# Optimization experiments

Measured on AMD Instinct MI355X. Metric: run time of the kernel, lower is better.

Reference implementation:

```python
import jax, jax.numpy as jnp
import numpy as np

QMAX = 127.0
QMIN = -128.0


def setup_inputs() -> dict:
    key = jax.random.key(0)
    k1, k2, k3 = jax.random.split(key, 3)
    B, N, D, O = 4, 4096, 2048, 2048
    x = jax.random.normal(k1, (B, N, D), dtype=jnp.float32)
    weight = jax.random.normal(k2, (O, D), dtype=jnp.float32)
    bias = jax.random.normal(k3, (O,), dtype=jnp.float32)
    return {"x": x, "weight": weight, "bias": bias}


def reference(x, weight, bias):
    # --- per-row symmetric int8 quantization of the weight [O, D] ---
    w_max = jnp.clip(jnp.max(jnp.abs(weight), axis=1, keepdims=True), 1e-8, None)
    w_scale = (w_max / QMAX)                     # [O, 1]
    w_q = jnp.clip(jnp.round(weight / w_scale), QMIN, QMAX).astype(jnp.int8)
    w_scale = w_scale.squeeze(1).astype(jnp.float32)  # [O]

    # --- dynamic per-row symmetric int8 quantization of x [B, N, D] ---
    x_max = jnp.max(jnp.abs(x), axis=2, keepdims=True)       # [B, N, 1]
    x_scale = jnp.maximum(x_max / QMAX, 1e-12)               # [B, N, 1]
    x_q = jnp.clip(jnp.round(x / x_scale), QMIN, QMAX).astype(jnp.int8)

    # --- int8 GEMM accumulated in int32: [B,N,D] x [O,D]^T -> [B,N,O] ---
    acc = jnp.einsum("bnd,od->bno", x_q.astype(jnp.int32), w_q.astype(jnp.int32))

    # --- dequantize with per-row activation scale and per-out-channel weight scale ---
    y = acc.astype(jnp.float32) * x_scale.astype(jnp.float32) * w_scale[None, None, :]
    y = y + bias
    return y.astype(x.dtype)
```

## Files before the change

kernel.cpp:

```cpp
#include <hip/hip_runtime.h>
#include <stdint.h>
#include <stddef.h>

typedef int v4i __attribute__((ext_vector_type(4)));

#define GLOAD_LDS16(g, l) __builtin_amdgcn_global_load_lds( \
    (const __attribute__((address_space(1))) void*)(g),     \
    (__attribute__((address_space(3))) void*)(l), 16, 0, 0)

__device__ __forceinline__ int pack4(float4 f, float s) {
    int a = (int)rintf(f.x / s); a = a < -128 ? -128 : (a > 127 ? 127 : a);
    int b = (int)rintf(f.y / s); b = b < -128 ? -128 : (b > 127 ? 127 : b);
    int c = (int)rintf(f.z / s); c = c < -128 ? -128 : (c > 127 ? 127 : c);
    int d = (int)rintf(f.w / s); d = d < -128 ? -128 : (d > 127 ? 127 : d);
    return (a & 255) | ((b & 255) << 8) | ((c & 255) << 16) | ((d & 255) << 24);
}

__global__ __launch_bounds__(256) void quant_both_2048(
    const float* __restrict__ x, signed char* __restrict__ xq,
    float* __restrict__ xs,
    const float* __restrict__ w, signed char* __restrict__ wq,
    float* __restrict__ wsc, int nx4)
{
    const int lane = threadIdx.x & 63;
    const bool isx = ((int)blockIdx.x < nx4);
    const int rb   = isx ? blockIdx.x : (blockIdx.x - nx4);
    const int row  = rb * 4 + (threadIdx.x >> 6);
    const float* in = isx ? x : w;
    signed char* q  = isx ? xq : wq;
    float* scales   = isx ? xs : wsc;
    const float floorv = isx ? 1e-12f : (1e-8f / 127.0f);
    const float* rp = in + (size_t)row * 2048;

    float4 v[8];
#pragma unroll
    for (int j = 0; j < 2; ++j) {
        const float4* p = (const float4*)(rp + j * 1024 + lane * 16);
#pragma unroll
        for (int i = 0; i < 4; ++i) v[j * 4 + i] = p[i];
    }
    float am = 0.0f;
#pragma unroll
    for (int i = 0; i < 8; ++i) {
        am = fmaxf(am, fabsf(v[i].x));
        am = fmaxf(am, fabsf(v[i].y));
        am = fmaxf(am, fabsf(v[i].z));
        am = fmaxf(am, fabsf(v[i].w));
    }
#pragma unroll
    for (int off = 32; off; off >>= 1) am = fmaxf(am, __shfl_xor(am, off));
    const float s = fmaxf(am / 127.0f, floorv);

#pragma unroll
    for (int j = 0; j < 2; ++j) {
        int4 pk;
        pk.x = pack4(v[j * 4 + 0], s);
        pk.y = pack4(v[j * 4 + 1], s);
        pk.z = pack4(v[j * 4 + 2], s);
        pk.w = pack4(v[j * 4 + 3], s);
        *(int4*)(q + (size_t)row * 2048 + j * 1024 + lane * 16) = pk;
    }
    if (lane == 0) scales[row] = s;
}

__global__ __launch_bounds__(256, 3) void gemm_i8_r3s(
    const signed char* __restrict__ xq, const signed char* __restrict__ wq,
    const float* __restrict__ xs, const float* __restrict__ ws,
    const float* __restrict__ bias, float* __restrict__ out, int K)
{
    __shared__ __align__(16) signed char lds[49152];

    const int tid  = threadIdx.x;
    const int lane = tid & 63;
    const int wid  = tid >> 6;
    const int wm   = wid >> 1;
    const int wn   = wid & 1;

    const int nwg  = gridDim.x * gridDim.y;
    int orig = blockIdx.y * gridDim.x + blockIdx.x;
    int swz  = ((nwg & 7) == 0) ? ((orig & 7) * (nwg >> 3) + (orig >> 3)) : orig;
    const int brow = (swz / gridDim.x) * 128;
    const int bcol = (swz % gridDim.x) * 128;

    const int gch = (((tid & 3) ^ ((tid >> 3) & 3)) << 4);
    const signed char* gA = xq + (size_t)(brow + (tid >> 2)) * K;
    const signed char* gB = wq + (size_t)(bcol + (tid >> 2)) * K;

#define ST4(tt, bb) do {                                                                  \
    GLOAD_LDS16(gA + (size_t)(tt) * 64 + gch,                  lds + (bb) * 16384 + (tid << 4));         \
    GLOAD_LDS16(gA + (size_t)64 * K + (size_t)(tt) * 64 + gch, lds + (bb) * 16384 + 4096 + (tid << 4));  \
    GLOAD_LDS16(gB + (size_t)(tt) * 64 + gch,                  lds + (bb) * 16384 + 8192 + (tid << 4));  \
    GLOAD_LDS16(gB + (size_t)64 * K + (size_t)(tt) * 64 + gch, lds + (bb) * 16384 + 12288 + (tid << 4)); \
} while (0)

    const int rl   = lane & 15;
    const int ko   = lane >> 4;
    const int slot = ((ko ^ ((rl >> 1) & 3)) << 4);

#define FRAG_A(bb, r) (*(const v4i*)(lds + (bb) * 16384 + (r) * 64 + slot))
#define FRAG_B(bb, r) (*(const v4i*)(lds + (bb) * 16384 + 8192 + (r) * 64 + slot))

    v4i acc[4][4] = {};
    const int ar = wm * 64 + rl;
    const int br = wn * 64 + rl;

    ST4(0, 0);
    ST4(1, 1);
    asm volatile("s_waitcnt vmcnt(4)" ::: "memory");
    __builtin_amdgcn_s_barrier();

    const int NT = K >> 6;
    for (int t = 0; t < NT; ++t) {
        const int buf = t % 3;

        v4i af[4], bf[4];
#pragma unroll
        for (int m = 0; m < 4; ++m) af[m] = FRAG_A(buf, ar + m * 16);
#pragma unroll
        for (int n = 0; n < 4; ++n) bf[n] = FRAG_B(buf, br + n * 16);

        if (t + 2 < NT) ST4(t + 2, (t + 2) % 3);

#pragma unroll
        for (int m = 0; m < 4; ++m)
#pragma unroll
            for (int n = 0; n < 4; ++n)
                acc[m][n] = __builtin_amdgcn_mfma_i32_16x16x64_i8(
                    af[m], bf[n], acc[m][n], 0, 0, 0);

        if (t + 2 < NT) {
            asm volatile("s_waitcnt vmcnt(4) lgkmcnt(0)" ::: "memory");
            __builtin_amdgcn_s_barrier();
        } else if (t + 2 == NT) {
            asm volatile("s_waitcnt vmcnt(0) lgkmcnt(0)" ::: "memory");
            __builtin_amdgcn_s_barrier();
        }
    }

    const int rg = lane >> 4;
#pragma unroll
    for (int n = 0; n < 4; ++n) {
        const int col = bcol + wn * 64 + n * 16 + rl;
        const float wsc = ws[col];
        const float bv  = bias[col];
#pragma unroll
        for (int m = 0; m < 4; ++m) {
#pragma unroll
            for (int j = 0; j < 4; ++j) {
                const int row = brow + wm * 64 + m * 16 + rg * 4 + j;
                out[(size_t)row * 2048 + col] =
                    (float)acc[m][n][j] * xs[row] * wsc + bv;
            }
        }
    }
#undef ST4
#undef FRAG_A
#undef FRAG_B
}

extern "C" void kernel_launch(void* const* d_in, const int* in_sizes, int n_in,
                              void* d_out, int out_size, void* d_ws, size_t ws_size,
                              hipStream_t stream) {
    const float* x    = (const float*)d_in[0];
    const float* w    = (const float*)d_in[1];
    const float* bias = (const float*)d_in[2];
    float* out = (float*)d_out;

    const int D = 2048;
    const int O = in_sizes[2];
    const int M = in_sizes[0] / D;

    char* wsb = (char*)d_ws;
    signed char* xq  = (signed char*)wsb;
    signed char* wqp = (signed char*)(wsb + (size_t)M * D);
    float* xs  = (float*)(wsb + (size_t)M * D + (size_t)O * D);
    float* wsc = (float*)(wsb + (size_t)M * D + (size_t)O * D + (size_t)M * 4);

    quant_both_2048<<<(M + O) / 4, 256, 0, stream>>>(x, xq, xs, w, wqp, wsc, M / 4);

    dim3 grid(O / 128, M / 128);
    gemm_i8_r3s<<<grid, 256, 0, stream>>>(xq, wqp, xs, wsc, bias, out, D);
}
```

Before: 131.1 us.

## Give each wave private LDS staging to eliminate block barriers in int8 GEMM

Each of the four waves now loads its own 64-row A and B slices into a private 32KB LDS region with a 4-stage ring, so no workgroup barriers are needed and only per-wave vmcnt waits gate consumption. Fragments are double-buffered in registers with the loop unrolled by two so that LDS reads overlap MFMAs. The cost is that A and B rows shared between waves are now loaded twice, which doubles global traffic per block, and the 128KB LDS footprint limits occupancy to one block per CU.

```diff
diff --git a/kernel.cpp b/kernel.cpp
--- a/kernel.cpp
+++ b/kernel.cpp
@@ -63,12 +63,12 @@
     if (lane == 0) scales[row] = s;
 }
 
-__global__ __launch_bounds__(256, 3) void gemm_i8_r3s(
+__global__ __launch_bounds__(256, 1) void gemm_i8_nobar(
     const signed char* __restrict__ xq, const signed char* __restrict__ wq,
     const float* __restrict__ xs, const float* __restrict__ ws,
     const float* __restrict__ bias, float* __restrict__ out, int K)
 {
-    __shared__ __align__(16) signed char lds[49152];
+    __shared__ __align__(16) signed char lds[131072];
 
     const int tid  = threadIdx.x;
     const int lane = tid & 63;
@@ -82,59 +82,91 @@
     const int brow = (swz / gridDim.x) * 128;
     const int bcol = (swz % gridDim.x) * 128;
 
-    const int gch = (((tid & 3) ^ ((tid >> 3) & 3)) << 4);
-    const signed char* gA = xq + (size_t)(brow + (tid >> 2)) * K;
-    const signed char* gB = wq + (size_t)(bcol + (tid >> 2)) * K;
-
-#define ST4(tt, bb) do {                                                                  \
-    GLOAD_LDS16(gA + (size_t)(tt) * 64 + gch,                  lds + (bb) * 16384 + (tid << 4));         \
-    GLOAD_LDS16(gA + (size_t)64 * K + (size_t)(tt) * 64 + gch, lds + (bb) * 16384 + 4096 + (tid << 4));  \
-    GLOAD_LDS16(gB + (size_t)(tt) * 64 + gch,                  lds + (bb) * 16384 + 8192 + (tid << 4));  \
-    GLOAD_LDS16(gB + (size_t)64 * K + (size_t)(tt) * 64 + gch, lds + (bb) * 16384 + 12288 + (tid << 4)); \
+    signed char* ldsW = lds + wid * 32768;
+
+    const int gch = (((lane & 3) ^ ((lane >> 3) & 3)) << 4);
+    const signed char* gAl = xq + (size_t)(brow + wm * 64 + (lane >> 2)) * K + gch;
+    const signed char* gBl = wq + (size_t)(bcol + wn * 64 + (lane >> 2)) * K + gch;
+
+#define ST8(tt, bb) do {                                                              \
+    GLOAD_LDS16(gAl + (size_t)(tt) * 64,                  ldsW + (bb) * 8192 + (lane << 4));         \
+    GLOAD_LDS16(gAl + (size_t)16 * K + (size_t)(tt) * 64, ldsW + (bb) * 8192 + 1024 + (lane << 4));  \
+    GLOAD_LDS16(gAl + (size_t)32 * K + (size_t)(tt) * 64, ldsW + (bb) * 8192 + 2048 + (lane << 4));  \
+    GLOAD_LDS16(gAl + (size_t)48 * K + (size_t)(tt) * 64, ldsW + (bb) * 8192 + 3072 + (lane << 4));  \
+    GLOAD_LDS16(gBl + (size_t)(tt) * 64,                  ldsW + (bb) * 8192 + 4096 + (lane << 4));  \
+    GLOAD_LDS16(gBl + (size_t)16 * K + (size_t)(tt) * 64, ldsW + (bb) * 8192 + 5120 + (lane << 4));  \
+    GLOAD_LDS16(gBl + (size_t)32 * K + (size_t)(tt) * 64, ldsW + (bb) * 8192 + 6144 + (lane << 4));  \
+    GLOAD_LDS16(gBl + (size_t)48 * K + (size_t)(tt) * 64, ldsW + (bb) * 8192 + 7168 + (lane << 4));  \
 } while (0)
 
     const int rl   = lane & 15;
     const int ko   = lane >> 4;
     const int slot = ((ko ^ ((rl >> 1) & 3)) << 4);
 
-#define FRAG_A(bb, r) (*(const v4i*)(lds + (bb) * 16384 + (r) * 64 + slot))
-#define FRAG_B(bb, r) (*(const v4i*)(lds + (bb) * 16384 + 8192 + (r) * 64 + slot))
+#define FRAG_A(bb, m) (*(const v4i*)(ldsW + (bb) * 8192 + ((m) * 16 + rl) * 64 + slot))
+#define FRAG_B(bb, n) (*(const v4i*)(ldsW + (bb) * 8192 + 4096 + ((n) * 16 + rl) * 64 + slot))
+
+#define MFMA16(A0, A1, A2, A3, B0, B1, B2, B3)                                              \
+    do {                                                                                    \
+        acc[0][0] = __builtin_amdgcn_mfma_i32_16x16x64_i8(A0, B0, acc[0][0], 0, 0, 0);      \
+        acc[0][1] = __builtin_amdgcn_mfma_i32_16x16x64_i8(A0, B1, acc[0][1], 0, 0, 0);      \
+        acc[0][2] = __builtin_amdgcn_mfma_i32_16x16x64_i8(A0, B2, acc[0][2], 0, 0, 0);      \
+        acc[0][3] = __builtin_amdgcn_mfma_i32_16x16x64_i8(A0, B3, acc[0][3], 0, 0, 0);      \
+        acc[1][0] = __builtin_amdgcn_mfma_i32_16x16x64_i8(A1, B0, acc[1][0], 0, 0, 0);      \
+        acc[1][1] = __builtin_amdgcn_mfma_i32_16x16x64_i8(A1, B1, acc[1][1], 0, 0, 0);      \
+        acc[1][2] = __builtin_amdgcn_mfma_i32_16x16x64_i8(A1, B2, acc[1][2], 0, 0, 0);      \
+        acc[1][3] = __builtin_amdgcn_mfma_i32_16x16x64_i8(A1, B3, acc[1][3], 0, 0, 0);      \
+        acc[2][0] = __builtin_amdgcn_mfma_i32_16x16x64_i8(A2, B0, acc[2][0], 0, 0, 0);      \
+        acc[2][1] = __builtin_amdgcn_mfma_i32_16x16x64_i8(A2, B1, acc[2][1], 0, 0, 0);      \
+        acc[2][2] = __builtin_amdgcn_mfma_i32_16x16x64_i8(A2, B2, acc[2][2], 0, 0, 0);      \
+        acc[2][3] = __builtin_amdgcn_mfma_i32_16x16x64_i8(A2, B3, acc[2][3], 0, 0, 0);      \
+        acc[3][0] = __builtin_amdgcn_mfma_i32_16x16x64_i8(A3, B0, acc[3][0], 0, 0, 0);      \
+        acc[3][1] = __builtin_amdgcn_mfma_i32_16x16x64_i8(A3, B1, acc[3][1], 0, 0, 0);      \
+        acc[3][2] = __builtin_amdgcn_mfma_i32_16x16x64_i8(A3, B2, acc[3][2], 0, 0, 0);      \
+        acc[3][3] = __builtin_amdgcn_mfma_i32_16x16x64_i8(A3, B3, acc[3][3], 0, 0, 0);      \
+    } while (0)
 
     v4i acc[4][4] = {};
-    const int ar = wm * 64 + rl;
-    const int br = wn * 64 + rl;
-
-    ST4(0, 0);
-    ST4(1, 1);
-    asm volatile("s_waitcnt vmcnt(4)" ::: "memory");
-    __builtin_amdgcn_s_barrier();
+
+    ST8(0, 0);
+    ST8(1, 1);
+    ST8(2, 2);
+    asm volatile("s_waitcnt vmcnt(16)" ::: "memory");
+    v4i cA0 = FRAG_A(0, 0), cA1 = FRAG_A(0, 1), cA2 = FRAG_A(0, 2), cA3 = FRAG_A(0, 3);
+    v4i cB0 = FRAG_B(0, 0), cB1 = FRAG_B(0, 1), cB2 = FRAG_B(0, 2), cB3 = FRAG_B(0, 3);
+    v4i nA0, nA1, nA2, nA3, nB0, nB1, nB2, nB3;
 
     const int NT = K >> 6;
-    for (int t = 0; t < NT; ++t) {
-        const int buf = t % 3;
-
-        v4i af[4], bf[4];
-#pragma unroll
-        for (int m = 0; m < 4; ++m) af[m] = FRAG_A(buf, ar + m * 16);
-#pragma unroll
-        for (int n = 0; n < 4; ++n) bf[n] = FRAG_B(buf, br + n * 16);
-
-        if (t + 2 < NT) ST4(t + 2, (t + 2) % 3);
-
-#pragma unroll
-        for (int m = 0; m < 4; ++m)
-#pragma unroll
-            for (int n = 0; n < 4; ++n)
-                acc[m][n] = __builtin_amdgcn_mfma_i32_16x16x64_i8(
-                    af[m], bf[n], acc[m][n], 0, 0, 0);
-
+    for (int t = 0; t < NT; t += 2) {
+        if (t + 3 < NT) {
+            ST8(t + 3, (t + 3) & 3);
+            asm volatile("s_waitcnt vmcnt(16)" ::: "memory");
+        } else {
+            asm volatile("s_waitcnt vmcnt(0)" ::: "memory");
+        }
+        {
+            const int nb = (t + 1) & 3;
+            nA0 = FRAG_A(nb, 0); nA1 = FRAG_A(nb, 1);
+            nA2 = FRAG_A(nb, 2); nA3 = FRAG_A(nb, 3);
+            nB0 = FRAG_B(nb, 0); nB1 = FRAG_B(nb, 1);
+            nB2 = FRAG_B(nb, 2); nB3 = FRAG_B(nb, 3);
+        }
+        MFMA16(cA0, cA1, cA2, cA3, cB0, cB1, cB2, cB3);
+
+        if (t + 4 < NT) {
+            ST8(t + 4, (t + 4) & 3);
+            asm volatile("s_waitcnt vmcnt(16)" ::: "memory");
+        } else if (t + 2 < NT) {
+            asm volatile("s_waitcnt vmcnt(8)" ::: "memory");
+        }
         if (t + 2 < NT) {
-            asm volatile("s_waitcnt vmcnt(4) lgkmcnt(0)" ::: "memory");
-            __builtin_amdgcn_s_barrier();
-        } else if (t + 2 == NT) {
-            asm volatile("s_waitcnt vmcnt(0) lgkmcnt(0)" ::: "memory");
-            __builtin_amdgcn_s_barrier();
-        }
+            const int cb = (t + 2) & 3;
+            cA0 = FRAG_A(cb, 0); cA1 = FRAG_A(cb, 1);
+            cA2 = FRAG_A(cb, 2); cA3 = FRAG_A(cb, 3);
+            cB0 = FRAG_B(cb, 0); cB1 = FRAG_B(cb, 1);
+            cB2 = FRAG_B(cb, 2); cB3 = FRAG_B(cb, 3);
+        }
+        MFMA16(nA0, nA1, nA2, nA3, nB0, nB1, nB2, nB3);
     }
 
     const int rg = lane >> 4;
@@ -153,9 +185,10 @@
             }
         }
     }
-#undef ST4
+#undef ST8
 #undef FRAG_A
 #undef FRAG_B
+#undef MFMA16
 }
 
 extern "C" void kernel_launch(void* const* d_in, const int* in_sizes, int n_in,
@@ -179,5 +212,5 @@
     quant_both_2048<<<(M + O) / 4, 256, 0, stream>>>(x, xq, xs, w, wqp, wsc, M / 4);
 
     dim3 grid(O / 128, M / 128);
-    gemm_i8_r3s<<<grid, 256, 0, stream>>>(xq, wqp, xs, wsc, bias, out, D);
-}
+    gemm_i8_nobar<<<grid, 256, 0, stream>>>(xq, wqp, xs, wsc, bias, out, D);
+}
```

Measured after the change: 155.3 us. 1.18x slower.
